# Performance work log

Measured on AMD Instinct MI355X. Metric: run time of the kernel, lower is better.

The kernel has to match this reference:

```python
import jax, jax.numpy as jnp
import numpy as np

B, S, D, H = 2, 2048, 1024, 16
HD = D // H  # head_dim = 64


def setup_inputs() -> dict:
    key = jax.random.key(0)
    k1, k2, k3, k4, k5 = jax.random.split(key, 5)
    x = jax.random.normal(k1, (B, S, D), dtype=jnp.float32)
    # causal additive mask [S, S]: 0 on/below diagonal, -1e9 above
    mask = jnp.where(jnp.tril(jnp.ones((S, S), dtype=bool)), 0.0, -1e9).astype(jnp.float32)
    scale = 1.0 / np.sqrt(D)
    W_qkv = jax.random.normal(k2, (D, 3 * D), dtype=jnp.float32) * scale
    b_qkv = jax.random.normal(k3, (3 * D,), dtype=jnp.float32) * 0.01
    W_o = jax.random.normal(k4, (D, D), dtype=jnp.float32) * scale
    b_o = jax.random.normal(k5, (D,), dtype=jnp.float32) * 0.01
    return {"x": x, "mask": mask, "W_qkv": W_qkv, "b_qkv": b_qkv, "W_o": W_o, "b_o": b_o}


def reference(x, mask, W_qkv, b_qkv, W_o, b_o):
    b, s, d = x.shape
    qkv = x @ W_qkv + b_qkv                         # [B,S,3D]
    qkv = qkv.reshape(b, s, H, 3 * HD).transpose(0, 2, 1, 3)  # [B,H,S,3*HD]
    q, k, v = jnp.split(qkv, 3, axis=-1)            # each [B,H,S,HD]
    scores = jnp.einsum('bhqd,bhkd->bhqk', q, k) / np.sqrt(HD)  # [B,H,S,S]
    scores = scores + mask                           # broadcast [S,S] additive mask
    attn = jax.nn.softmax(scores, axis=-1)
    vals = jnp.einsum('bhqk,bhkd->bhqd', attn, v)    # [B,H,S,HD]
    vals = vals.transpose(0, 2, 1, 3).reshape(b, s, d)
    return vals @ W_o + b_o
```

## Files before the change

kernel.cpp:

```cpp
#include <hip/hip_runtime.h>

#define NB 2
#define NS 2048
#define ND 1024
#define NH 16
#define NHD 64
#define QLD (3 * ND)
#define PADP 72
#define PADV 68

typedef unsigned short u16;
typedef __attribute__((ext_vector_type(8))) short short8;
typedef __attribute__((ext_vector_type(4))) short short4v;
typedef __attribute__((ext_vector_type(4))) float f32x4;

__device__ __forceinline__ u16 f2b(float f) {
    unsigned int x = __float_as_uint(f);
    return (u16)((x + 0x7fffu + ((x >> 16) & 1u)) >> 16);
}

__device__ __forceinline__ unsigned int cvtpk(float lo, float hi) {
    unsigned int r;
    asm("v_cvt_pk_bf16_f32 %0, %1, %2" : "=v"(r) : "v"(lo), "v"(hi));
    return r;
}

__global__ __launch_bounds__(256) void prep(
    const float* __restrict__ x, u16* __restrict__ x_bf,
    const float* __restrict__ Wqkv, u16* __restrict__ WqkvT,
    const float* __restrict__ Wo, u16* __restrict__ WoT)
{
    __shared__ u16 Ts[64 * 72];
    const int bid = blockIdx.x;
    const int t = threadIdx.x;

    if (bid < 2048) {
        const int i = (bid * 256 + t) * 8;
        float4 a = *(const float4*)(x + i);
        float4 b = *(const float4*)(x + i + 4);
        *(ushort4*)(x_bf + i)     = make_ushort4(f2b(a.x), f2b(a.y), f2b(a.z), f2b(a.w));
        *(ushort4*)(x_bf + i + 4) = make_ushort4(f2b(b.x), f2b(b.y), f2b(b.z), f2b(b.w));
        return;
    }

    const float* W; u16* WT; int N, bx, by;
    if (bid < 2048 + 768) {
        const int r = bid - 2048;
        W = Wqkv; WT = WqkvT; N = QLD; bx = r % 48; by = r / 48;
    } else {
        const int r = bid - 2816;
        W = Wo; WT = WoT; N = ND; bx = r & 15; by = r >> 4;
    }
    const int K = ND;
    const int k0 = by << 6, n0 = bx << 6;
    const int rr0 = t >> 4, c = (t & 15) << 2;
    #pragma unroll
    for (int rr = 0; rr < 64; rr += 16) {
        float4 v = *(const float4*)&W[(size_t)(k0 + rr0 + rr) * N + n0 + c];
        Ts[(c + 0) * 72 + rr0 + rr] = f2b(v.x);
        Ts[(c + 1) * 72 + rr0 + rr] = f2b(v.y);
        Ts[(c + 2) * 72 + rr0 + rr] = f2b(v.z);
        Ts[(c + 3) * 72 + rr0 + rr] = f2b(v.w);
    }
    __syncthreads();
    const int n = t >> 2, cc = (t & 3) << 4;
    uint4 a = *(const uint4*)&Ts[n * 72 + cc];
    uint4 b = *(const uint4*)&Ts[n * 72 + cc + 8];
    *(uint4*)&WT[(size_t)(n0 + n) * K + k0 + cc]     = a;
    *(uint4*)&WT[(size_t)(n0 + n) * K + k0 + cc + 8] = b;
}

template <int BN, bool STORE_BF16>
__global__ __launch_bounds__(256) void gemm_mfma(
    const u16* __restrict__ A, const u16* __restrict__ BT,
    const float* __restrict__ bias,
    void* __restrict__ C, int M, int N, int K)
{
    constexpr int BIS = BN / 64;
    constexpr int NJ  = BN / 32;
    __shared__ u16 As[128 * 32];
    __shared__ u16 Bs[BN * 32];

    const int tid = threadIdx.x;
    const int wave = tid >> 6, lane = tid & 63;
    const int col = lane & 15, quad = lane >> 4;
    const int wm = wave >> 1, wn = wave & 1;

    const int nwgx = gridDim.x;
    const int wg = blockIdx.y * nwgx + blockIdx.x;
    const int cpx = (nwgx * gridDim.y) >> 3;
    const int swz = (wg & 7) * cpx + (wg >> 3);
    const int row0 = (swz / nwgx) << 7, col0 = (swz % nwgx) * BN;

    f32x4 acc[4][NJ] = {};

    const u16* asrc[2];
    u16* adst[2];
    #pragma unroll
    for (int is = 0; is < 2; ++is) {
        const int J = is * 256 + wave * 64 + lane;
        const int m = J >> 2;
        const int q = (J & 3) ^ ((m >> 1) & 3);
        asrc[is] = A + (size_t)(row0 + m) * K + q * 8;
        adst[is] = &As[(size_t)(is * 256 + wave * 64) * 8];
    }
    const u16* bsrc[BIS];
    u16* bdst[BIS];
    #pragma unroll
    for (int is = 0; is < BIS; ++is) {
        const int J = is * 256 + wave * 64 + lane;
        const int m = J >> 2;
        const int q = (J & 3) ^ ((m >> 1) & 3);
        bsrc[is] = BT + (size_t)(col0 + m) * K + q * 8;
        bdst[is] = &Bs[(size_t)(is * 256 + wave * 64) * 8];
    }

    for (int kk = 0; kk < K; kk += 32) {
        __syncthreads();
        #pragma unroll
        for (int is = 0; is < 2; ++is)
            __builtin_amdgcn_global_load_lds(
                (const __attribute__((address_space(1))) unsigned int*)(asrc[is] + kk),
                (__attribute__((address_space(3))) unsigned int*)adst[is], 16, 0, 0);
        #pragma unroll
        for (int is = 0; is < BIS; ++is)
            __builtin_amdgcn_global_load_lds(
                (const __attribute__((address_space(1))) unsigned int*)(bsrc[is] + kk),
                (__attribute__((address_space(3))) unsigned int*)bdst[is], 16, 0, 0);
        __syncthreads();

        short8 af[4], bf[NJ];
        #pragma unroll
        for (int i = 0; i < 4; ++i) {
            const int m = wm * 64 + i * 16 + col;
            af[i] = *(const short8*)&As[(m * 4 + (quad ^ ((m >> 1) & 3))) * 8];
        }
        #pragma unroll
        for (int j = 0; j < NJ; ++j) {
            const int n = wn * (BN / 2) + j * 16 + col;
            bf[j] = *(const short8*)&Bs[(n * 4 + (quad ^ ((n >> 1) & 3))) * 8];
        }
        #pragma unroll
        for (int i = 0; i < 4; ++i)
            #pragma unroll
            for (int j = 0; j < NJ; ++j)
                acc[i][j] = __builtin_amdgcn_mfma_f32_16x16x32_bf16(
                    af[i], bf[j], acc[i][j], 0, 0, 0);
    }

    #pragma unroll
    for (int j = 0; j < NJ; ++j) {
        const int gc = col0 + wn * (BN / 2) + j * 16 + col;
        const float bj = bias[gc];
        #pragma unroll
        for (int i = 0; i < 4; ++i) {
            const int gr = row0 + wm * 64 + i * 16 + quad * 4;
            #pragma unroll
            for (int r = 0; r < 4; ++r) {
                const float v = acc[i][j][r] + bj;
                if (STORE_BF16)
                    ((u16*)C)[(size_t)(gr + r) * N + gc] = f2b(v);
                else
                    ((float*)C)[(size_t)(gr + r) * N + gc] = v;
            }
        }
    }
}

__global__ __launch_bounds__(256) void attn_kernel(
    const u16* __restrict__ qkv, u16* __restrict__ vals)
{
    __shared__ u16 Ks[2][64 * 64];
    __shared__ u16 Vt[2][64 * PADV];
    __shared__ u16 Ps[64 * PADP];

    const int tid = threadIdx.x;
    const int wave = tid >> 6, lane = tid & 63;
    const int col = lane & 15, quad = lane >> 4;
    const int qtA = blockIdx.x;
    const int qtB = 31 - qtA;
    const int bh = blockIdx.y;
    const int b = bh >> 4, h = bh & 15;
    const size_t base = (size_t)b * NS * QLD + (size_t)h * (3 * NHD);
    const int qloc = wave * 16 + col;

    int Jrow[2], Jcol[2];
    #pragma unroll
    for (int is = 0; is < 2; ++is) {
        const int J = is * 256 + wave * 64 + lane;
        Jrow[is] = J >> 3;
        Jcol[is] = ((J & 7) ^ (Jrow[is] & 7)) << 3;
    }

    auto stage_tile = [&](int buf, int srow, int coloff) {
        #pragma unroll
        for (int is = 0; is < 2; ++is) {
            __builtin_amdgcn_global_load_lds(
                (const __attribute__((address_space(1))) unsigned int*)
                    (qkv + base + (size_t)(srow + Jrow[is]) * QLD + coloff + Jcol[is]),
                (__attribute__((address_space(3))) unsigned int*)
                    &Ks[buf][(size_t)(is * 256 + wave * 64) * 8], 16, 0, 0);
        }
    };
    auto read_frag = [&](int buf, int row, int half) -> short8 {
        const int blk = row * 8 + ((quad + (half << 2)) ^ (row & 7));
        return *(const short8*)&Ks[buf][blk << 3];
    };

    const int vtx = tid & 15, vty = tid >> 4;
    const int vk0 = vty << 2, vd0 = vtx << 2;
    auto load_vregs = [&](int kt, ushort4* vr) {
        const u16* vsrc = qkv + base + (size_t)(kt * 64 + vk0) * QLD + 2 * NHD + vd0;
        vr[0] = *(const ushort4*)(vsrc);
        vr[1] = *(const ushort4*)(vsrc + QLD);
        vr[2] = *(const ushort4*)(vsrc + 2 * QLD);
        vr[3] = *(const ushort4*)(vsrc + 3 * QLD);
    };
    auto write_vt = [&](int buf, const ushort4* vr) {
        *(ushort4*)&Vt[buf][(vd0 + 0) * PADV + vk0] =
            make_ushort4(vr[0].x, vr[1].x, vr[2].x, vr[3].x);
        *(ushort4*)&Vt[buf][(vd0 + 1) * PADV + vk0] =
            make_ushort4(vr[0].y, vr[1].y, vr[2].y, vr[3].y);
        *(ushort4*)&Vt[buf][(vd0 + 2) * PADV + vk0] =
            make_ushort4(vr[0].z, vr[1].z, vr[2].z, vr[3].z);
        *(ushort4*)&Vt[buf][(vd0 + 3) * PADV + vk0] =
            make_ushort4(vr[0].w, vr[1].w, vr[2].w, vr[3].w);
    };

    stage_tile(0, qtA * 64, 0);
    stage_tile(1, qtB * 64, 0);
    __syncthreads();
    short8 bqA0 = read_frag(0, qloc, 0), bqA1 = read_frag(0, qloc, 1);
    short8 bqB0 = read_frag(1, qloc, 0), bqB1 = read_frag(1, qloc, 1);
    __syncthreads();

    f32x4 accA[4] = {}, accB[4] = {};
    float mA = -1e30f, lA = 0.f, mB = -1e30f, lB = 0.f;

    auto qk = [&](const short8& b0, const short8& b1,
                  short8 (&kb)[4][2], f32x4 (&s)[4]) {
        __builtin_amdgcn_s_setprio(1);
        #pragma unroll
        for (int kg = 0; kg < 4; ++kg) {
            s[kg] = __builtin_amdgcn_mfma_f32_16x16x32_bf16(kb[kg][0], b0, s[kg], 0, 0, 0);
            s[kg] = __builtin_amdgcn_mfma_f32_16x16x32_bf16(kb[kg][1], b1, s[kg], 0, 0, 0);
        }
        __builtin_amdgcn_s_setprio(0);
    };

    auto sm = [&](f32x4 (&s)[4], f32x4 (&acc)[4], float& m, float& l, bool diag) {
        #pragma unroll
        for (int kg = 0; kg < 4; ++kg)
            #pragma unroll
            for (int r = 0; r < 4; ++r) {
                float v = s[kg][r] * 0.125f;
                if (diag && (kg * 16 + quad * 4 + r > qloc)) v = -1e30f;
                s[kg][r] = v;
            }
        float mx = -1e30f;
        #pragma unroll
        for (int kg = 0; kg < 4; ++kg)
            mx = fmaxf(mx, fmaxf(fmaxf(s[kg][0], s[kg][1]), fmaxf(s[kg][2], s[kg][3])));
        mx = fmaxf(mx, __shfl_xor(mx, 16, 64));
        mx = fmaxf(mx, __shfl_xor(mx, 32, 64));
        if (!__all(mx <= m + 8.f)) {
            const float mn = fmaxf(m, mx);
            const float alpha = __expf(m - mn);
            m = mn;
            l *= alpha;
            #pragma unroll
            for (int dg = 0; dg < 4; ++dg)
                #pragma unroll
                for (int r = 0; r < 4; ++r) acc[dg][r] *= alpha;
        }
        float psum = 0.f;
        #pragma unroll
        for (int kg = 0; kg < 4; ++kg) {
            float p0 = __expf(s[kg][0] - m);
            float p1 = __expf(s[kg][1] - m);
            float p2 = __expf(s[kg][2] - m);
            float p3 = __expf(s[kg][3] - m);
            psum += (p0 + p1) + (p2 + p3);
            uint2 w;
            w.x = cvtpk(p0, p1);
            w.y = cvtpk(p2, p3);
            *(uint2*)&Ps[qloc * PADP + kg * 16 + quad * 4] = w;
        }
        psum += __shfl_xor(psum, 16, 64);
        psum += __shfl_xor(psum, 32, 64);
        l += psum;
    };

    auto pv = [&](short8 (&vb)[4][2], f32x4 (&acc)[4]) {
        short8 pb0 = *(const short8*)&Ps[qloc * PADP + quad * 8];
        short8 pb1 = *(const short8*)&Ps[qloc * PADP + 32 + quad * 8];
        __builtin_amdgcn_s_setprio(1);
        #pragma unroll
        for (int dg = 0; dg < 4; ++dg) {
            acc[dg] = __builtin_amdgcn_mfma_f32_16x16x32_bf16(vb[dg][0], pb0, acc[dg], 0, 0, 0);
            acc[dg] = __builtin_amdgcn_mfma_f32_16x16x32_bf16(vb[dg][1], pb1, acc[dg], 0, 0, 0);
        }
        __builtin_amdgcn_s_setprio(0);
    };

    ushort4 vr[4];
    stage_tile(0, 0, NHD);
    load_vregs(0, vr);
    write_vt(0, vr);

    for (int kt = 0; kt <= qtB; ++kt) {
        const int cur = kt & 1, nxt = cur ^ 1;
        __syncthreads();
        if (kt < qtB) {
            stage_tile(nxt, (kt + 1) * 64, NHD);
            load_vregs(kt + 1, vr);
        }

        short8 kb[4][2], vb[4][2];
        #pragma unroll
        for (int kg = 0; kg < 4; ++kg) {
            kb[kg][0] = read_frag(cur, kg * 16 + col, 0);
            kb[kg][1] = read_frag(cur, kg * 16 + col, 1);
        }
        #pragma unroll
        for (int dg = 0; dg < 4; ++dg) {
            const int n = dg * 16 + col;
            short4v lo0 = *(const short4v*)&Vt[cur][n * PADV + quad * 8];
            short4v hi0 = *(const short4v*)&Vt[cur][n * PADV + quad * 8 + 4];
            short4v lo1 = *(const short4v*)&Vt[cur][n * PADV + 32 + quad * 8];
            short4v hi1 = *(const short4v*)&Vt[cur][n * PADV + 32 + quad * 8 + 4];
            vb[dg][0] = __builtin_shufflevector(lo0, hi0, 0, 1, 2, 3, 4, 5, 6, 7);
            vb[dg][1] = __builtin_shufflevector(lo1, hi1, 0, 1, 2, 3, 4, 5, 6, 7);
        }

        {
            f32x4 s[4] = {};
            qk(bqB0, bqB1, kb, s);
            sm(s, accB, mB, lB, kt == qtB);
            pv(vb, accB);
        }
        if (kt <= qtA) {
            f32x4 s[4] = {};
            qk(bqA0, bqA1, kb, s);
            sm(s, accA, mA, lA, kt == qtA);
            pv(vb, accA);
        }

        if (kt < qtB) write_vt(nxt, vr);
    }

    {
        const float inv = 1.f / lA;
        const size_t rowoff = ((size_t)b * NS + qtA * 64 + qloc) * ND + h * NHD;
        #pragma unroll
        for (int dg = 0; dg < 4; ++dg) {
            uint2 o;
            o.x = cvtpk(accA[dg][0] * inv, accA[dg][1] * inv);
            o.y = cvtpk(accA[dg][2] * inv, accA[dg][3] * inv);
            *(uint2*)(vals + rowoff + dg * 16 + quad * 4) = o;
        }
    }
    {
        const float inv = 1.f / lB;
        const size_t rowoff = ((size_t)b * NS + qtB * 64 + qloc) * ND + h * NHD;
        #pragma unroll
        for (int dg = 0; dg < 4; ++dg) {
            uint2 o;
            o.x = cvtpk(accB[dg][0] * inv, accB[dg][1] * inv);
            o.y = cvtpk(accB[dg][2] * inv, accB[dg][3] * inv);
            *(uint2*)(vals + rowoff + dg * 16 + quad * 4) = o;
        }
    }
}

extern "C" void kernel_launch(void* const* d_in, const int* in_sizes, int n_in,
                              void* d_out, int out_size, void* d_ws, size_t ws_size,
                              hipStream_t stream)
{
    const float* x    = (const float*)d_in[0];
    const float* Wqkv = (const float*)d_in[2];
    const float* bqkv = (const float*)d_in[3];
    const float* Wo   = (const float*)d_in[4];
    const float* bo   = (const float*)d_in[5];
    float* out = (float*)d_out;

    u16* x_bf   = (u16*)d_ws;
    u16* WqkvT  = x_bf   + (size_t)4096 * 1024;
    u16* WoT    = WqkvT  + (size_t)3072 * 1024;
    u16* qkv    = WoT    + (size_t)1024 * 1024;
    u16* vals   = qkv    + (size_t)4096 * 3072;

    const int M = NB * NS;

    prep<<<dim3(2048 + 768 + 256), dim3(256), 0, stream>>>(
        x, x_bf, Wqkv, WqkvT, Wo, WoT);

    gemm_mfma<128, true><<<dim3(QLD / 128, M / 128), dim3(256), 0, stream>>>(
        x_bf, WqkvT, bqkv, qkv, M, QLD, ND);
    attn_kernel<<<dim3(16, NB * NH), dim3(256), 0, stream>>>(qkv, vals);
    gemm_mfma<64, false><<<dim3(ND / 64, M / 128), dim3(256), 0, stream>>>(
        vals, WoT, bo, out, M, ND, ND);
}
```

Before: 210.8 us.

## Double GEMM K-step to 64, swizzle V tile in LDS, interleave attention tiles

The GEMM kernel now stages 64-wide K slices per iteration with an 8-chunk XOR swizzle, which halves the number of barrier pairs and global-to-LDS rounds but doubles LDS use per block. In attention, the padded transposed-V buffer is replaced by an unpadded, XOR-swizzled layout so each B fragment is one 16-byte LDS read instead of four 8-byte reads. The two query tiles' QK, softmax and PV steps are also interleaved so the second tile's MFMAs can overlap the first tile's softmax.

Result: slower. 216.8 us (+2.8%).

```diff
diff --git a/kernel.cpp b/kernel.cpp
--- a/kernel.cpp
+++ b/kernel.cpp
@@ -7,11 +7,9 @@
 #define NHD 64
 #define QLD (3 * ND)
 #define PADP 72
-#define PADV 68
 
 typedef unsigned short u16;
 typedef __attribute__((ext_vector_type(8))) short short8;
-typedef __attribute__((ext_vector_type(4))) short short4v;
 typedef __attribute__((ext_vector_type(4))) float f32x4;
 
 __device__ __forceinline__ u16 f2b(float f) {
@@ -23,6 +21,10 @@
     unsigned int r;
     asm("v_cvt_pk_bf16_f32 %0, %1, %2" : "=v"(r) : "v"(lo), "v"(hi));
     return r;
+}
+
+__device__ __forceinline__ int swz8(int d) {
+    return ((d >> 1) ^ (d >> 3)) & 7;
 }
 
 __global__ __launch_bounds__(256) void prep(
@@ -76,10 +78,11 @@
     const float* __restrict__ bias,
     void* __restrict__ C, int M, int N, int K)
 {
-    constexpr int BIS = BN / 64;
+    constexpr int AIS = 4;
+    constexpr int BIS = BN / 32;
     constexpr int NJ  = BN / 32;
-    __shared__ u16 As[128 * 32];
-    __shared__ u16 Bs[BN * 32];
+    __shared__ u16 As[128 * 64];
+    __shared__ u16 Bs[BN * 64];
 
     const int tid = threadIdx.x;
     const int wave = tid >> 6, lane = tid & 63;
@@ -94,13 +97,13 @@
 
     f32x4 acc[4][NJ] = {};
 
-    const u16* asrc[2];
-    u16* adst[2];
+    const u16* asrc[AIS];
+    u16* adst[AIS];
     #pragma unroll
-    for (int is = 0; is < 2; ++is) {
+    for (int is = 0; is < AIS; ++is) {
         const int J = is * 256 + wave * 64 + lane;
-        const int m = J >> 2;
-        const int q = (J & 3) ^ ((m >> 1) & 3);
+        const int m = J >> 3;
+        const int q = (J & 7) ^ swz8(m);
         asrc[is] = A + (size_t)(row0 + m) * K + q * 8;
         adst[is] = &As[(size_t)(is * 256 + wave * 64) * 8];
     }
@@ -109,16 +112,16 @@
     #pragma unroll
     for (int is = 0; is < BIS; ++is) {
         const int J = is * 256 + wave * 64 + lane;
-        const int m = J >> 2;
-        const int q = (J & 3) ^ ((m >> 1) & 3);
+        const int m = J >> 3;
+        const int q = (J & 7) ^ swz8(m);
         bsrc[is] = BT + (size_t)(col0 + m) * K + q * 8;
         bdst[is] = &Bs[(size_t)(is * 256 + wave * 64) * 8];
     }
 
-    for (int kk = 0; kk < K; kk += 32) {
+    for (int kk = 0; kk < K; kk += 64) {
         __syncthreads();
         #pragma unroll
-        for (int is = 0; is < 2; ++is)
+        for (int is = 0; is < AIS; ++is)
             __builtin_amdgcn_global_load_lds(
                 (const __attribute__((address_space(1))) unsigned int*)(asrc[is] + kk),
                 (__attribute__((address_space(3))) unsigned int*)adst[is], 16, 0, 0);
@@ -129,23 +132,26 @@
                 (__attribute__((address_space(3))) unsigned int*)bdst[is], 16, 0, 0);
         __syncthreads();
 
-        short8 af[4], bf[NJ];
-        #pragma unroll
-        for (int i = 0; i < 4; ++i) {
-            const int m = wm * 64 + i * 16 + col;
-            af[i] = *(const short8*)&As[(m * 4 + (quad ^ ((m >> 1) & 3))) * 8];
-        }
-        #pragma unroll
-        for (int j = 0; j < NJ; ++j) {
-            const int n = wn * (BN / 2) + j * 16 + col;
-            bf[j] = *(const short8*)&Bs[(n * 4 + (quad ^ ((n >> 1) & 3))) * 8];
-        }
-        #pragma unroll
-        for (int i = 0; i < 4; ++i)
-            #pragma unroll
-            for (int j = 0; j < NJ; ++j)
-                acc[i][j] = __builtin_amdgcn_mfma_f32_16x16x32_bf16(
-                    af[i], bf[j], acc[i][j], 0, 0, 0);
+        #pragma unroll
+        for (int h = 0; h < 2; ++h) {
+            short8 af[4], bf[NJ];
+            #pragma unroll
+            for (int i = 0; i < 4; ++i) {
+                const int m = wm * 64 + i * 16 + col;
+                af[i] = *(const short8*)&As[(m * 8 + ((4 * h + quad) ^ swz8(m))) * 8];
+            }
+            #pragma unroll
+            for (int j = 0; j < NJ; ++j) {
+                const int n = wn * (BN / 2) + j * 16 + col;
+                bf[j] = *(const short8*)&Bs[(n * 8 + ((4 * h + quad) ^ swz8(n))) * 8];
+            }
+            #pragma unroll
+            for (int i = 0; i < 4; ++i)
+                #pragma unroll
+                for (int j = 0; j < NJ; ++j)
+                    acc[i][j] = __builtin_amdgcn_mfma_f32_16x16x32_bf16(
+                        af[i], bf[j], acc[i][j], 0, 0, 0);
+        }
     }
 
     #pragma unroll
@@ -171,7 +177,7 @@
     const u16* __restrict__ qkv, u16* __restrict__ vals)
 {
     __shared__ u16 Ks[2][64 * 64];
-    __shared__ u16 Vt[2][64 * PADV];
+    __shared__ u16 Vt[2][64 * 64];
     __shared__ u16 Ps[64 * PADP];
 
     const int tid = threadIdx.x;
@@ -216,15 +222,17 @@
         vr[2] = *(const ushort4*)(vsrc + 2 * QLD);
         vr[3] = *(const ushort4*)(vsrc + 3 * QLD);
     };
+    const int vC = vty >> 1, vS = (vty & 1) << 2;
     auto write_vt = [&](int buf, const ushort4* vr) {
-        *(ushort4*)&Vt[buf][(vd0 + 0) * PADV + vk0] =
-            make_ushort4(vr[0].x, vr[1].x, vr[2].x, vr[3].x);
-        *(ushort4*)&Vt[buf][(vd0 + 1) * PADV + vk0] =
-            make_ushort4(vr[0].y, vr[1].y, vr[2].y, vr[3].y);
-        *(ushort4*)&Vt[buf][(vd0 + 2) * PADV + vk0] =
-            make_ushort4(vr[0].z, vr[1].z, vr[2].z, vr[3].z);
-        *(ushort4*)&Vt[buf][(vd0 + 3) * PADV + vk0] =
-            make_ushort4(vr[0].w, vr[1].w, vr[2].w, vr[3].w);
+        #pragma unroll
+        for (int i = 0; i < 4; ++i) {
+            const int d = vd0 + i;
+            u16* p = &Vt[buf][d * 64 + ((vC ^ swz8(d)) << 3) + vS];
+            *(ushort4*)p = make_ushort4(((const u16*)&vr[0])[i],
+                                        ((const u16*)&vr[1])[i],
+                                        ((const u16*)&vr[2])[i],
+                                        ((const u16*)&vr[3])[i]);
+        }
     };
 
     stage_tile(0, qtA * 64, 0);
@@ -325,25 +333,25 @@
         #pragma unroll
         for (int dg = 0; dg < 4; ++dg) {
             const int n = dg * 16 + col;
-            short4v lo0 = *(const short4v*)&Vt[cur][n * PADV + quad * 8];
-            short4v hi0 = *(const short4v*)&Vt[cur][n * PADV + quad * 8 + 4];
-            short4v lo1 = *(const short4v*)&Vt[cur][n * PADV + 32 + quad * 8];
-            short4v hi1 = *(const short4v*)&Vt[cur][n * PADV + 32 + quad * 8 + 4];
-            vb[dg][0] = __builtin_shufflevector(lo0, hi0, 0, 1, 2, 3, 4, 5, 6, 7);
-            vb[dg][1] = __builtin_shufflevector(lo1, hi1, 0, 1, 2, 3, 4, 5, 6, 7);
+            #pragma unroll
+            for (int c = 0; c < 2; ++c)
+                vb[dg][c] = *(const short8*)
+                    &Vt[cur][n * 64 + (((4 * c + quad) ^ swz8(n)) << 3)];
         }
 
         {
-            f32x4 s[4] = {};
-            qk(bqB0, bqB1, kb, s);
-            sm(s, accB, mB, lB, kt == qtB);
-            pv(vb, accB);
-        }
-        if (kt <= qtA) {
-            f32x4 s[4] = {};
-            qk(bqA0, bqA1, kb, s);
-            sm(s, accA, mA, lA, kt == qtA);
-            pv(vb, accA);
+            f32x4 sB[4] = {};
+            qk(bqB0, bqB1, kb, sB);
+            sm(sB, accB, mB, lB, kt == qtB);
+            if (kt <= qtA) {
+                f32x4 sA[4] = {};
+                qk(bqA0, bqA1, kb, sA);
+                pv(vb, accB);
+                sm(sA, accA, mA, lA, kt == qtA);
+                pv(vb, accA);
+            } else {
+                pv(vb, accB);
+            }
         }
 
         if (kt < qtB) write_vt(nxt, vr);
```
